# Kernel tuning notes

Measured on AMD Instinct MI355X. Metric: run time of the kernel, lower is better.

## Reference

```python
import jax, jax.numpy as jnp
import numpy as np

B, K, D = 128, 2048, 512   # batch, out_features (classes), in_features
C = 1.0                    # curvature c


def setup_inputs() -> dict:
    key = jax.random.key(0)
    k1, k2, k3 = jax.random.split(key, 3)
    # inputs must lie strictly inside the Poincare ball of radius 1/sqrt(c)
    v = jax.random.normal(k1, (B, D), jnp.float32)
    inp = v * (0.7 / (1.0 + jnp.linalg.norm(v, axis=-1, keepdims=True)))
    # p is a hyperbolic parameter (init zeros in the module; use small in-ball
    # values here so the math is non-degenerate)
    pv = jax.random.normal(k2, (K, D), jnp.float32)
    p = pv * (0.3 / (1.0 + jnp.linalg.norm(pv, axis=-1, keepdims=True)))
    # a is Euclidean, xavier-uniform scale ~ 1/sqrt(D)
    a = jax.random.normal(k3, (K, D), jnp.float32) * (1.0 / np.sqrt(D))
    return {"inp": inp, "p": p, "a": a}


def hyperbolic_logits(inp, p, a, c):
    """Ganea et al. hyperbolic MLR logits.

    logit_k(x) = (lambda_{p_k} ||a_k|| / sqrt(c))
                 * asinh( 2 sqrt(c) <(-p_k) (+)_c x, a_k>
                          / ((1 - c ||(-p_k)(+)_c x||^2) ||a_k||) )
    """
    c = jnp.float32(c)
    sc = jnp.sqrt(c)
    u = -p                                   # [K,D]
    uv = jnp.einsum('bd,kd->bk', inp, u)     # <u_k, x_b>
    uu = jnp.sum(u * u, -1)                  # [K]
    vv = jnp.sum(inp * inp, -1)              # [B]
    # Mobius addition w = u (+)_c x, broadcast to [B,K,D]
    alpha = 1.0 + 2.0 * c * uv + c * vv[:, None]          # coeff of u
    beta = 1.0 - c * uu[None, :]                           # coeff of x
    den = 1.0 + 2.0 * c * uv + (c * c) * uu[None, :] * vv[:, None]
    w = (alpha[..., None] * u[None, :, :]
         + beta[..., None] * inp[:, None, :]) / den[..., None]   # [B,K,D]
    ww = jnp.sum(w * w, -1)                  # [B,K]
    wa = jnp.einsum('bkd,kd->bk', w, a)      # [B,K]
    a_norm = jnp.linalg.norm(a, axis=-1)     # [K]
    lam_p = 2.0 / (1.0 - c * jnp.sum(p * p, -1))   # conformal factor at p_k
    num = 2.0 * sc * wa
    denom = a_norm[None, :] * (1.0 - c * ww)
    return (lam_p * a_norm / sc)[None, :] * jnp.arcsinh(num / denom)  # [B,K]


def reference(inp, p, a):
    return hyperbolic_logits(inp, p, a, C)
```

## Files before the change

kernel.cpp:

```cpp
#include <hip/hip_runtime.h>
#include <hip/hip_bf16.h>

#define B_SZ 128
#define K_SZ 2048
#define D_SZ 512
#define ROWP 520

typedef __attribute__((ext_vector_type(8))) short short8;
typedef __attribute__((ext_vector_type(4))) float floatx4;

static __device__ inline unsigned short f2b(float f) {
  unsigned int u = __float_as_uint(f);
  return (unsigned short)((u + 0x7fffu + ((u >> 16) & 1u)) >> 16);
}

__global__ __launch_bounds__(256, 2) void fused_kernel(
    const float* __restrict__ x, const float* __restrict__ p,
    const float* __restrict__ a, float* __restrict__ out) {
  __shared__ unsigned short xs[32 * ROWP];
  __shared__ unsigned short ps[16 * ROWP];
  __shared__ unsigned short as_[16 * ROWP];
  __shared__ float stats[32 + 48];

  const int t = threadIdx.x;
  const int bm = (blockIdx.x >> 7) * 32;
  const int kn = (blockIdx.x & 127) * 16;

  {
    const int r = t >> 3, s = t & 7;
    const float4* src = (const float4*)(x + (size_t)(bm + r) * D_SZ);
    float vvp = 0.f;
#pragma unroll
    for (int i = 0; i < 16; ++i) {
      float4 v = src[s + i * 8];
      vvp += v.x * v.x + v.y * v.y + v.z * v.z + v.w * v.w;
      ushort4 c;
      c.x = f2b(v.x); c.y = f2b(v.y); c.z = f2b(v.z); c.w = f2b(v.w);
      *(ushort4*)&xs[r * ROWP + (s + i * 8) * 4] = c;
    }
    vvp += __shfl_xor(vvp, 1, 64);
    vvp += __shfl_xor(vvp, 2, 64);
    vvp += __shfl_xor(vvp, 4, 64);
    if (s == 0) stats[r] = vvp;
  }

  {
    const int r = t >> 4, s = t & 15;
    const float4* sp = (const float4*)(p + (size_t)(kn + r) * D_SZ);
    const float4* sa = (const float4*)(a + (size_t)(kn + r) * D_SZ);
    float pp = 0.f, pa = 0.f, aa = 0.f;
#pragma unroll
    for (int i = 0; i < 8; ++i) {
      float4 pv = sp[s + i * 16];
      float4 av = sa[s + i * 16];
      pp += pv.x * pv.x + pv.y * pv.y + pv.z * pv.z + pv.w * pv.w;
      pa += pv.x * av.x + pv.y * av.y + pv.z * av.z + pv.w * av.w;
      aa += av.x * av.x + av.y * av.y + av.z * av.z + av.w * av.w;
      ushort4 pc, ac;
      pc.x = f2b(pv.x); pc.y = f2b(pv.y); pc.z = f2b(pv.z); pc.w = f2b(pv.w);
      ac.x = f2b(av.x); ac.y = f2b(av.y); ac.z = f2b(av.z); ac.w = f2b(av.w);
      *(ushort4*)&ps[r * ROWP + (s + i * 16) * 4] = pc;
      *(ushort4*)&as_[r * ROWP + (s + i * 16) * 4] = ac;
    }
    pp += __shfl_xor(pp, 1, 64);
    pa += __shfl_xor(pa, 1, 64);
    aa += __shfl_xor(aa, 1, 64);
    pp += __shfl_xor(pp, 2, 64);
    pa += __shfl_xor(pa, 2, 64);
    aa += __shfl_xor(aa, 2, 64);
    pp += __shfl_xor(pp, 4, 64);
    pa += __shfl_xor(pa, 4, 64);
    aa += __shfl_xor(aa, 4, 64);
    pp += __shfl_xor(pp, 8, 64);
    pa += __shfl_xor(pa, 8, 64);
    aa += __shfl_xor(aa, 8, 64);
    if (s == 0) {
      stats[32 + r] = pp;
      stats[48 + r] = -pa;
      stats[64 + r] = sqrtf(aa);
    }
  }
  __syncthreads();

  const int w = t >> 6, lane = t & 63;
  const int row16 = lane & 15, quad = lane >> 4;
  const int wm = w & 1, dh = w >> 1;
  const unsigned short* xrow = &xs[(wm * 16 + row16) * ROWP + dh * 256 + quad * 8];
  const unsigned short* prow = &ps[row16 * ROWP + dh * 256 + quad * 8];
  const unsigned short* arow = &as_[row16 * ROWP + dh * 256 + quad * 8];
  floatx4 cs = {0.f, 0.f, 0.f, 0.f};
  floatx4 ca = {0.f, 0.f, 0.f, 0.f};
#pragma unroll
  for (int dc = 0; dc < 8; ++dc) {
    short8 af = *(const short8*)(xrow + dc * 32);
    short8 bp = *(const short8*)(prow + dc * 32);
    short8 bv = *(const short8*)(arow + dc * 32);
    cs = __builtin_amdgcn_mfma_f32_16x16x32_bf16(af, bp, cs, 0, 0, 0);
    ca = __builtin_amdgcn_mfma_f32_16x16x32_bf16(af, bv, ca, 0, 0, 0);
  }

  __syncthreads();
  float* part_s = (float*)ps;
  float* part_a = part_s + 1024;
  *(floatx4*)&part_s[(w * 64 + lane) * 4] = cs;
  *(floatx4*)&part_a[(w * 64 + lane) * 4] = ca;
  __syncthreads();

#pragma unroll
  for (int o = 0; o < 2; ++o) {
    const int idx = t + o * 256;
    const int m16 = idx >> 4;
    const int n = idx & 15;
    const int wmI = m16 >> 4, mr = m16 & 15;
    const int lsrc = ((mr >> 2) << 4) | n;
    const int reg = mr & 3;
    const float sdot = part_s[(wmI * 64 + lsrc) * 4 + reg] +
                       part_s[((2 + wmI) * 64 + lsrc) * 4 + reg];
    const float adot = part_a[(wmI * 64 + lsrc) * 4 + reg] +
                       part_a[((2 + wmI) * 64 + lsrc) * 4 + reg];
    const float vvb = stats[m16];
    const float uuk = stats[32 + n];
    const float nuak = stats[48 + n];
    const float ank = stats[64 + n];
    const float beta = 1.f - uuk;
    const float scale = (2.f / beta) * ank;
    const float uv = -sdot;
    const float alpha = 1.f + 2.f * uv + vvb;
    const float den = 1.f + 2.f * uv + uuk * vvb;
    const float inv = 1.f / den;
    const float wwn =
        (alpha * alpha * uuk + 2.f * alpha * beta * uv + beta * beta * vvb) *
        inv * inv;
    const float wa = (alpha * nuak + beta * adot) * inv;
    const float z = 2.f * wa / (ank * (1.f - wwn));
    out[(size_t)(bm + m16) * K_SZ + (kn + n)] = scale * asinhf(z);
  }
}

extern "C" void kernel_launch(void* const* d_in, const int* in_sizes, int n_in,
                              void* d_out, int out_size, void* d_ws, size_t ws_size,
                              hipStream_t stream) {
  const float* x = (const float*)d_in[0];
  const float* p = (const float*)d_in[1];
  const float* a = (const float*)d_in[2];
  float* out = (float*)d_out;
  (void)d_ws; (void)ws_size;

  fused_kernel<<<(B_SZ / 32) * (K_SZ / 16), 256, 0, stream>>>(x, p, a, out);
}
```

Measured before the change: 66.94 us.

## Split into prep kernel for bf16 conversion and stats, then MFMA kernel

Adds a prep kernel that converts x, p and a to bf16 once into the workspace and computes the per-row norms and p·a dot products. The main kernel then reads the bf16 operands straight from global memory into MFMA fragments, with no LDS staging. This removes the redundant fp32 reloads and conversions, since each of the 512 blocks previously re-read and converted its x, p and a tiles. The cost is a second launch plus an extra global round trip through the workspace.

```diff
diff --git a/kernel.cpp b/kernel.cpp
--- a/kernel.cpp
+++ b/kernel.cpp
@@ -1,10 +1,8 @@
 #include <hip/hip_runtime.h>
-#include <hip/hip_bf16.h>
 
 #define B_SZ 128
 #define K_SZ 2048
 #define D_SZ 512
-#define ROWP 520
 
 typedef __attribute__((ext_vector_type(8))) short short8;
 typedef __attribute__((ext_vector_type(4))) float floatx4;
@@ -14,80 +12,93 @@
   return (unsigned short)((u + 0x7fffu + ((u >> 16) & 1u)) >> 16);
 }
 
-__global__ __launch_bounds__(256, 2) void fused_kernel(
+static __device__ inline ushort4 cvt4(float4 v) {
+  ushort4 c;
+  c.x = f2b(v.x); c.y = f2b(v.y); c.z = f2b(v.z); c.w = f2b(v.w);
+  return c;
+}
+
+__global__ __launch_bounds__(256) void prep_kernel(
     const float* __restrict__ x, const float* __restrict__ p,
-    const float* __restrict__ a, float* __restrict__ out) {
-  __shared__ unsigned short xs[32 * ROWP];
-  __shared__ unsigned short ps[16 * ROWP];
-  __shared__ unsigned short as_[16 * ROWP];
-  __shared__ float stats[32 + 48];
+    const float* __restrict__ a, unsigned short* __restrict__ xb,
+    unsigned short* __restrict__ pb, unsigned short* __restrict__ ab,
+    float* __restrict__ stats) {
+  const int wid = (blockIdx.x << 2) + (threadIdx.x >> 6);
+  const int lane = threadIdx.x & 63;
+  if (wid < K_SZ) {
+    const float4* sp = (const float4*)(p + (size_t)wid * D_SZ);
+    const float4* sa = (const float4*)(a + (size_t)wid * D_SZ);
+    float4 p0 = sp[lane], p1 = sp[lane + 64];
+    float4 a0 = sa[lane], a1 = sa[lane + 64];
+    float pp = p0.x * p0.x + p0.y * p0.y + p0.z * p0.z + p0.w * p0.w +
+               p1.x * p1.x + p1.y * p1.y + p1.z * p1.z + p1.w * p1.w;
+    float pa = p0.x * a0.x + p0.y * a0.y + p0.z * a0.z + p0.w * a0.w +
+               p1.x * a1.x + p1.y * a1.y + p1.z * a1.z + p1.w * a1.w;
+    float aa = a0.x * a0.x + a0.y * a0.y + a0.z * a0.z + a0.w * a0.w +
+               a1.x * a1.x + a1.y * a1.y + a1.z * a1.z + a1.w * a1.w;
+    unsigned short* pr = pb + (size_t)wid * D_SZ;
+    unsigned short* ar = ab + (size_t)wid * D_SZ;
+    *(ushort4*)(pr + lane * 4) = cvt4(p0);
+    *(ushort4*)(pr + 256 + lane * 4) = cvt4(p1);
+    *(ushort4*)(ar + lane * 4) = cvt4(a0);
+    *(ushort4*)(ar + 256 + lane * 4) = cvt4(a1);
+#pragma unroll
+    for (int off = 32; off; off >>= 1) {
+      pp += __shfl_xor(pp, off, 64);
+      pa += __shfl_xor(pa, off, 64);
+      aa += __shfl_xor(aa, off, 64);
+    }
+    if (lane == 0) {
+      stats[B_SZ + wid] = pp;
+      stats[B_SZ + K_SZ + wid] = -pa;
+      stats[B_SZ + 2 * K_SZ + wid] = sqrtf(aa);
+    }
+  } else {
+    const int b = wid - K_SZ;
+    const float4* sx = (const float4*)(x + (size_t)b * D_SZ);
+    float4 v0 = sx[lane], v1 = sx[lane + 64];
+    float vv = v0.x * v0.x + v0.y * v0.y + v0.z * v0.z + v0.w * v0.w +
+               v1.x * v1.x + v1.y * v1.y + v1.z * v1.z + v1.w * v1.w;
+    unsigned short* xr = xb + (size_t)b * D_SZ;
+    *(ushort4*)(xr + lane * 4) = cvt4(v0);
+    *(ushort4*)(xr + 256 + lane * 4) = cvt4(v1);
+#pragma unroll
+    for (int off = 32; off; off >>= 1) vv += __shfl_xor(vv, off, 64);
+    if (lane == 0) stats[b] = vv;
+  }
+}
 
+__global__ __launch_bounds__(256, 2) void mlr_kernel(
+    const unsigned short* __restrict__ xb, const unsigned short* __restrict__ pb,
+    const unsigned short* __restrict__ ab, const float* __restrict__ stats,
+    float* __restrict__ out) {
+  __shared__ float part[2048];
   const int t = threadIdx.x;
-  const int bm = (blockIdx.x >> 7) * 32;
-  const int kn = (blockIdx.x & 127) * 16;
-
-  {
-    const int r = t >> 3, s = t & 7;
-    const float4* src = (const float4*)(x + (size_t)(bm + r) * D_SZ);
-    float vvp = 0.f;
-#pragma unroll
-    for (int i = 0; i < 16; ++i) {
-      float4 v = src[s + i * 8];
-      vvp += v.x * v.x + v.y * v.y + v.z * v.z + v.w * v.w;
-      ushort4 c;
-      c.x = f2b(v.x); c.y = f2b(v.y); c.z = f2b(v.z); c.w = f2b(v.w);
-      *(ushort4*)&xs[r * ROWP + (s + i * 8) * 4] = c;
-    }
-    vvp += __shfl_xor(vvp, 1, 64);
-    vvp += __shfl_xor(vvp, 2, 64);
-    vvp += __shfl_xor(vvp, 4, 64);
-    if (s == 0) stats[r] = vvp;
-  }
-
-  {
-    const int r = t >> 4, s = t & 15;
-    const float4* sp = (const float4*)(p + (size_t)(kn + r) * D_SZ);
-    const float4* sa = (const float4*)(a + (size_t)(kn + r) * D_SZ);
-    float pp = 0.f, pa = 0.f, aa = 0.f;
-#pragma unroll
-    for (int i = 0; i < 8; ++i) {
-      float4 pv = sp[s + i * 16];
-      float4 av = sa[s + i * 16];
-      pp += pv.x * pv.x + pv.y * pv.y + pv.z * pv.z + pv.w * pv.w;
-      pa += pv.x * av.x + pv.y * av.y + pv.z * av.z + pv.w * av.w;
-      aa += av.x * av.x + av.y * av.y + av.z * av.z + av.w * av.w;
-      ushort4 pc, ac;
-      pc.x = f2b(pv.x); pc.y = f2b(pv.y); pc.z = f2b(pv.z); pc.w = f2b(pv.w);
-      ac.x = f2b(av.x); ac.y = f2b(av.y); ac.z = f2b(av.z); ac.w = f2b(av.w);
-      *(ushort4*)&ps[r * ROWP + (s + i * 16) * 4] = pc;
-      *(ushort4*)&as_[r * ROWP + (s + i * 16) * 4] = ac;
-    }
-    pp += __shfl_xor(pp, 1, 64);
-    pa += __shfl_xor(pa, 1, 64);
-    aa += __shfl_xor(aa, 1, 64);
-    pp += __shfl_xor(pp, 2, 64);
-    pa += __shfl_xor(pa, 2, 64);
-    aa += __shfl_xor(aa, 2, 64);
-    pp += __shfl_xor(pp, 4, 64);
-    pa += __shfl_xor(pa, 4, 64);
-    aa += __shfl_xor(aa, 4, 64);
-    pp += __shfl_xor(pp, 8, 64);
-    pa += __shfl_xor(pa, 8, 64);
-    aa += __shfl_xor(aa, 8, 64);
-    if (s == 0) {
-      stats[32 + r] = pp;
-      stats[48 + r] = -pa;
-      stats[64 + r] = sqrtf(aa);
-    }
-  }
-  __syncthreads();
-
+  const int mt = blockIdx.x >> 7;
+  const int kt = blockIdx.x & 127;
   const int w = t >> 6, lane = t & 63;
   const int row16 = lane & 15, quad = lane >> 4;
   const int wm = w & 1, dh = w >> 1;
-  const unsigned short* xrow = &xs[(wm * 16 + row16) * ROWP + dh * 256 + quad * 8];
-  const unsigned short* prow = &ps[row16 * ROWP + dh * 256 + quad * 8];
-  const unsigned short* arow = &as_[row16 * ROWP + dh * 256 + quad * 8];
+
+  const unsigned short* xrow =
+      xb + (size_t)(mt * 32 + wm * 16 + row16) * D_SZ + dh * 256 + quad * 8;
+  const unsigned short* prow =
+      pb + (size_t)(kt * 16 + row16) * D_SZ + dh * 256 + quad * 8;
+  const unsigned short* arow =
+      ab + (size_t)(kt * 16 + row16) * D_SZ + dh * 256 + quad * 8;
+
+  const int bm = mt * 32, kn = kt * 16;
+  float vvb[2], uuk[2], nuak[2], ank[2];
+#pragma unroll
+  for (int o = 0; o < 2; ++o) {
+    const int idx = t + o * 256;
+    const int m16 = idx >> 4, n = idx & 15;
+    vvb[o] = stats[bm + m16];
+    uuk[o] = stats[B_SZ + kn + n];
+    nuak[o] = stats[B_SZ + K_SZ + kn + n];
+    ank[o] = stats[B_SZ + 2 * K_SZ + kn + n];
+  }
+
   floatx4 cs = {0.f, 0.f, 0.f, 0.f};
   floatx4 ca = {0.f, 0.f, 0.f, 0.f};
 #pragma unroll
@@ -99,11 +110,10 @@
     ca = __builtin_amdgcn_mfma_f32_16x16x32_bf16(af, bv, ca, 0, 0, 0);
   }
 
-  __syncthreads();
-  float* part_s = (float*)ps;
-  float* part_a = part_s + 1024;
-  *(floatx4*)&part_s[(w * 64 + lane) * 4] = cs;
-  *(floatx4*)&part_a[(w * 64 + lane) * 4] = ca;
+  float* part_s = part;
+  float* part_a = part + 1024;
+  *(floatx4*)&part_s[t * 4] = cs;
+  *(floatx4*)&part_a[t * 4] = ca;
   __syncthreads();
 
 #pragma unroll
@@ -118,21 +128,16 @@
                        part_s[((2 + wmI) * 64 + lsrc) * 4 + reg];
     const float adot = part_a[(wmI * 64 + lsrc) * 4 + reg] +
                        part_a[((2 + wmI) * 64 + lsrc) * 4 + reg];
-    const float vvb = stats[m16];
-    const float uuk = stats[32 + n];
-    const float nuak = stats[48 + n];
-    const float ank = stats[64 + n];
-    const float beta = 1.f - uuk;
-    const float scale = (2.f / beta) * ank;
+    const float beta = 1.f - uuk[o];
+    const float scale = (2.f / beta) * ank[o];
     const float uv = -sdot;
-    const float alpha = 1.f + 2.f * uv + vvb;
-    const float den = 1.f + 2.f * uv + uuk * vvb;
+    const float alpha = 1.f + 2.f * uv + vvb[o];
+    const float den = 1.f + 2.f * uv + uuk[o] * vvb[o];
     const float inv = 1.f / den;
-    const float wwn =
-        (alpha * alpha * uuk + 2.f * alpha * beta * uv + beta * beta * vvb) *
-        inv * inv;
-    const float wa = (alpha * nuak + beta * adot) * inv;
-    const float z = 2.f * wa / (ank * (1.f - wwn));
+    const float wwn = (alpha * alpha * uuk[o] + 2.f * alpha * beta * uv +
+                       beta * beta * vvb[o]) * inv * inv;
+    const float wa = (alpha * nuak[o] + beta * adot) * inv;
+    const float z = 2.f * wa / (ank[o] * (1.f - wwn));
     out[(size_t)(bm + m16) * K_SZ + (kn + n)] = scale * asinhf(z);
   }
 }
@@ -144,7 +149,12 @@
   const float* p = (const float*)d_in[1];
   const float* a = (const float*)d_in[2];
   float* out = (float*)d_out;
-  (void)d_ws; (void)ws_size;
 
-  fused_kernel<<<(B_SZ / 32) * (K_SZ / 16), 256, 0, stream>>>(x, p, a, out);
+  unsigned short* xb = (unsigned short*)d_ws;
+  unsigned short* pb = xb + (size_t)B_SZ * D_SZ;
+  unsigned short* ab = pb + (size_t)K_SZ * D_SZ;
+  float* stats = (float*)(ab + (size_t)K_SZ * D_SZ);
+
+  prep_kernel<<<(K_SZ + B_SZ) / 4, 256, 0, stream>>>(x, p, a, xb, pb, ab, stats);
+  mlr_kernel<<<(B_SZ / 32) * (K_SZ / 16), 256, 0, stream>>>(xb, pb, ab, stats, out);
 }
```

New measurement: 69.85 us. 4.3% more time.
